# Kernel tuning notes

Measured on AMD Instinct MI355X. Metric: run time of the kernel, lower is better.

The kernel has to match this reference:

```python
import jax, jax.numpy as jnp
import numpy as np

# Brevitas-style fake quantization:
#  - Int8ActPerTensorFloat: signed, symmetric, per-tensor float scale, range [-128, 127]
#  - 4-bit weight, narrow range: [-7, 7]
#  - Int32Bias: quantized at scale s_in * s_w
# Scales are taken from per-tensor abs-max statistics (brevitas stats-based init).

def _round(v):
    return jnp.round(v)

def _fake_quant(v, scale, qmin, qmax):
    return jnp.clip(_round(v / scale), qmin, qmax) * scale


def setup_inputs() -> dict:
    key = jax.random.key(0)
    k1, k2, k3 = jax.random.split(key, 3)
    x = jax.random.normal(k1, (16, 3, 224, 224), dtype=jnp.float32)
    W = jax.random.normal(k2, (128, 3, 3, 3), dtype=jnp.float32) * 0.1
    b = jax.random.normal(k3, (128,), dtype=jnp.float32) * 0.01
    return {"x": x, "W": W, "b": b}


def reference(x, W, b):
    EPS = 1e-8
    # input quant: int8 per-tensor
    s_in = jnp.maximum(jnp.max(jnp.abs(x)) / 127.0, EPS)
    x_q = _fake_quant(x, s_in, -128.0, 127.0)
    # weight quant: 4-bit narrow-range per-tensor
    s_w = jnp.maximum(jnp.max(jnp.abs(W)) / 7.0, EPS)
    w_q = _fake_quant(W, s_w, -7.0, 7.0)
    # bias quant: int32 at scale s_in * s_w
    s_b = s_in * s_w
    b_q = _fake_quant(b, s_b, -2147483648.0, 2147483647.0)
    # conv2d, NCHW x OIHW -> NCHW, stride 1, valid padding (torch default padding=0)
    y = jax.lax.conv_general_dilated(
        x_q, w_q, window_strides=(1, 1), padding="VALID",
        dimension_numbers=("NCHW", "OIHW", "NCHW"))
    y = y + b_q[None, :, None, None]
    # output quant: int8 per-tensor
    s_out = jnp.maximum(jnp.max(jnp.abs(y)) / 127.0, EPS)
    y_q = _fake_quant(y, s_out, -128.0, 127.0)
    return y_q
```

## Files before the change

kernel.cpp:

```cpp
#include <hip/hip_runtime.h>
#include <stdint.h>

#define QEPS 1e-8f

typedef __bf16 bf16x8 __attribute__((ext_vector_type(8)));
typedef unsigned short ushortx8 __attribute__((ext_vector_type(8)));
typedef float floatx4 __attribute__((ext_vector_type(4)));


__global__ void k_init(unsigned int* s) { if (threadIdx.x < 4) s[threadIdx.x] = 0u; }

__global__ __launch_bounds__(256) void k_absmax(
    const float4* __restrict__ x, int n4,
    const float* __restrict__ W, int nw,
    unsigned int* __restrict__ s) {
  __shared__ unsigned int red[256];
  const int t = threadIdx.x;
  unsigned int m = 0u;
  const int i = blockIdx.x * 256 + t;
  if (i < n4) {
    float4 v = x[i];
    m =        __float_as_uint(v.x) & 0x7fffffffu;
    m = max(m, __float_as_uint(v.y) & 0x7fffffffu);
    m = max(m, __float_as_uint(v.z) & 0x7fffffffu);
    m = max(m, __float_as_uint(v.w) & 0x7fffffffu);
  }
  red[t] = m;
  __syncthreads();
  for (int off = 128; off > 0; off >>= 1) {
    if (t < off) red[t] = max(red[t], red[t + off]);
    __syncthreads();
  }
  if (t == 0) atomicMax(&s[0], red[0]);

  if (blockIdx.x == 0) {
    unsigned int mw = 0u;
    for (int j = t; j < nw; j += 256)
      mw = max(mw, __float_as_uint(W[j]) & 0x7fffffffu);
    __syncthreads();
    red[t] = mw;
    __syncthreads();
    for (int off = 128; off > 0; off >>= 1) {
      if (t < off) red[t] = max(red[t], red[t + off]);
      __syncthreads();
    }
    if (t == 0) atomicMax(&s[1], red[0]);
  }
}

#define OFF_XL  8320
#define OFF_QBL 16992
#define OFF_RED 17504
#define OFF_OL  18528
#define SMEM_P0 18528
#define SMEM_P1 47712

template<int PASS>
__global__ __launch_bounds__(256) void k_conv(
    const float* __restrict__ x, const float* __restrict__ W,
    const float* __restrict__ b, float* __restrict__ out,
    unsigned int* __restrict__ s) {
  extern __shared__ __align__(16) char smem[];
  unsigned short* const wl   = (unsigned short*)smem;
  unsigned short* const xl   = (unsigned short*)(smem + OFF_XL);
  float*          const qbl  = (float*)(smem + OFF_QBL);
  float*          const redf = (float*)(smem + OFF_RED);
  unsigned int*   const ol32 = (unsigned int*)(smem + OFF_OL);

  const int t = threadIdx.x;
  const float s_in = fmaxf(__uint_as_float(s[0]) / 127.0f, QEPS);
  const float s_w  = fmaxf(__uint_as_float(s[1]) / 7.0f,  QEPS);
  const float s_b  = s_in * s_w;

  float s_out = 1.0f, h = 1.0f;
  if (PASS == 1) {
    const float vmax = __uint_as_float(s[2]);
    s_out = fmaxf((s_b * vmax) / 127.0f, QEPS);
    h = s_b / s_out;
  }

  for (int i = t; i < 3456; i += 256) {
    const int o = i / 27;
    const int k = i - o * 27;
    float q = rintf(W[i] / s_w);
    q = fminf(fmaxf(q, -7.0f), 7.0f);
    wl[k * 130 + o] = (unsigned short)(__float_as_uint(q) >> 16);
  }
  for (int i = t; i < 5 * 130; i += 256) wl[27 * 130 + i] = 0;
  if (t < 128) qbl[t] = rintf(b[t] / s_b);
  for (int i = t; i < 72; i += 256) xl[(i >> 2) * 228 + 224 + (i & 3)] = 0;
  for (int i = t; i < 228; i += 256) xl[18 * 228 + i] = 0;

  #pragma unroll
  for (int sl = 0; sl < 2; ++sl) {
    const int R = blockIdx.x + sl * 1776;
    const int n = R / 222, oh = R - n * 222;
    for (int i = t; i < 9 * 224; i += 256) {
      const int row = i / 224;
      const int col = i - row * 224;
      const int c = row / 3, kh = row - c * 3;
      const float xv = x[((n * 3 + c) * 224 + (oh + kh)) * 224 + col];
      float q = fminf(fmaxf(rintf(xv / s_in), -128.0f), 127.0f);
      xl[(sl * 9 + row) * 228 + col] = (unsigned short)(__float_as_uint(q) >> 16);
    }
  }
  __syncthreads();

  const int lane = t & 63;
  const int wv = t >> 6;
  const int p = lane & 15;
  const int g = lane >> 4;

  bf16x8 bvw[8];
  #pragma unroll
  for (int tt8 = 0; tt8 < 8; ++tt8) {
    ushortx8 u;
    #pragma unroll
    for (int j = 0; j < 8; ++j)
      u[j] = wl[(g * 8 + j) * 130 + tt8 * 16 + p];
    bvw[tt8] = __builtin_bit_cast(bf16x8, u);
  }
  float qbp[8];
  #pragma unroll
  for (int tt8 = 0; tt8 < 8; ++tt8) qbp[tt8] = qbl[tt8 * 16 + p];

  float vmax_local = 0.0f;

  #pragma unroll
  for (int sl = 0; sl < 2; ++sl) {
    int off2[8];
    #pragma unroll
    for (int j = 0; j < 8; ++j) {
      const int k = g * 8 + j;
      int row, kw;
      if (k < 27) {
        const int c = k / 9, rem = k - c * 9;
        const int kh = rem / 3;
        kw = rem - kh * 3;
        row = sl * 9 + c * 3 + kh;
      } else { row = 18; kw = 0; }
      off2[j] = (row * 228 + kw) * 2;
    }

    const int R = blockIdx.x + sl * 1776;
    const int nn = R / 222, ohh = R - nn * 222;

    #pragma unroll 1
    for (int tt = wv; tt < 14; tt += 4) {
      const int ow0 = tt * 16;
      const char* xbase = (const char*)xl + (ow0 + p) * 2;

      ushortx8 bu;
      #pragma unroll
      for (int j = 0; j < 8; ++j)
        bu[j] = *(const unsigned short*)(xbase + off2[j]);
      const bf16x8 av = __builtin_bit_cast(bf16x8, bu);

      floatx4 acc[8];
      #pragma unroll
      for (int tt8 = 0; tt8 < 8; ++tt8) {
        const float qb = qbp[tt8];
        acc[tt8][0] = qb; acc[tt8][1] = qb; acc[tt8][2] = qb; acc[tt8][3] = qb;
      }
      #pragma unroll
      for (int tt8 = 0; tt8 < 8; ++tt8)
        acc[tt8] = __builtin_amdgcn_mfma_f32_16x16x32_bf16(av, bvw[tt8], acc[tt8], 0, 0, 0);

      if (PASS == 0) {
        #pragma unroll
        for (int tt8 = 0; tt8 < 8; ++tt8)
          #pragma unroll
          for (int r = 0; r < 4; ++r)
            vmax_local = fmaxf(vmax_local,
                (ow0 + 4 * g + r < 222) ? fabsf(acc[tt8][r]) : 0.0f);
      } else {
        #pragma unroll
        for (int tt8 = 0; tt8 < 8; ++tt8) {
          unsigned int pk = 0;
          #pragma unroll
          for (int r = 0; r < 4; ++r) {
            float q = rintf(acc[tt8][r] * h);
            q = fminf(fmaxf(q, -128.0f), 127.0f);
            pk |= ((unsigned int)((int)q & 255)) << (8 * r);
          }
          ol32[(tt8 * 16 + p) * 57 + (ow0 >> 2) + g] = pk;
        }
      }
    }

    if (PASS == 1) {
      __syncthreads();
      #pragma unroll 1
      for (int oc = wv * 32; oc < wv * 32 + 32; ++oc) {
        const unsigned int* src = ol32 + oc * 57;
        float* dst = out + (((nn * 128 + oc) * 222 + ohh) * 222);
        if (lane < 56) {
          const unsigned int bc = src[lane];
          if ((ohh & 1) == 0) {
            float f0 = (float)((int)(bc << 24) >> 24) * s_out;
            float f1 = (float)((int)(bc << 16) >> 24) * s_out;
            float f2 = (float)((int)(bc <<  8) >> 24) * s_out;
            float f3 = (float)((int) bc        >> 24) * s_out;
            if (lane < 55) *(float4*)(dst + 4 * lane) = make_float4(f0, f1, f2, f3);
            else           *(float2*)(dst + 220)      = make_float2(f0, f1);
          } else {
            if (lane == 0) {
              float f0 = (float)((int)(bc << 24) >> 24) * s_out;
              float f1 = (float)((int)(bc << 16) >> 24) * s_out;
              *(float2*)dst = make_float2(f0, f1);
            } else {
              const unsigned int ap = src[lane - 1];
              const unsigned int v = (ap >> 16) | (bc << 16);
              float f0 = (float)((int)(v << 24) >> 24) * s_out;
              float f1 = (float)((int)(v << 16) >> 24) * s_out;
              float f2 = (float)((int)(v <<  8) >> 24) * s_out;
              float f3 = (float)((int) v        >> 24) * s_out;
              *(float4*)(dst + 4 * lane - 2) = make_float4(f0, f1, f2, f3);
            }
          }
        }
      }
      __syncthreads();
    }
  }

  if (PASS == 0) {
    redf[t] = vmax_local;
    __syncthreads();
    for (int off = 128; off > 0; off >>= 1) {
      if (t < off) redf[t] = fmaxf(redf[t], redf[t + off]);
      __syncthreads();
    }
    if (t == 0) atomicMax(&s[2], __float_as_uint(redf[0]));
  }
}

extern "C" void kernel_launch(void* const* d_in, const int* in_sizes, int n_in,
                              void* d_out, int out_size, void* d_ws, size_t ws_size,
                              hipStream_t stream) {
  const float* x = (const float*)d_in[0];
  const float* W = (const float*)d_in[1];
  const float* b = (const float*)d_in[2];
  float* out = (float*)d_out;
  unsigned int* s = (unsigned int*)d_ws;

  k_init<<<1, 64, 0, stream>>>(s);

  const int n4 = in_sizes[0] / 4;
  k_absmax<<<(n4 + 255) / 256, 256, 0, stream>>>(
      (const float4*)x, n4, W, in_sizes[1], s);

  k_conv<0><<<1776, 256, SMEM_P0, stream>>>(x, W, b, out, s);
  k_conv<1><<<1776, 256, SMEM_P1, stream>>>(x, W, b, out, s);
}
```

Measured before the change: 574.1 us.

## Cache int16 conv accumulators in workspace instead of recomputing conv in second pass

```diff
diff --git a/kernel.cpp b/kernel.cpp
--- a/kernel.cpp
+++ b/kernel.cpp
@@ -45,6 +45,189 @@
       __syncthreads();
     }
     if (t == 0) atomicMax(&s[1], red[0]);
+  }
+}
+
+__global__ __launch_bounds__(256) void k_conv_ws(
+    const float* __restrict__ x, const float* __restrict__ W,
+    const float* __restrict__ b, unsigned short* __restrict__ y16,
+    unsigned int* __restrict__ s) {
+  __shared__ __align__(16) unsigned short wl[32 * 130];
+  __shared__ __align__(16) unsigned short xl[19 * 228];
+  __shared__ __align__(16) float qbl[128];
+  __shared__ float redf[256];
+
+  const int t = threadIdx.x;
+  const float s_in = fmaxf(__uint_as_float(s[0]) / 127.0f, QEPS);
+  const float s_w  = fmaxf(__uint_as_float(s[1]) / 7.0f,  QEPS);
+  const float s_b  = s_in * s_w;
+
+  for (int i = t; i < 3456; i += 256) {
+    const int o = i / 27;
+    const int k = i - o * 27;
+    float q = rintf(W[i] / s_w);
+    q = fminf(fmaxf(q, -7.0f), 7.0f);
+    wl[k * 130 + o] = (unsigned short)(__float_as_uint(q) >> 16);
+  }
+  for (int i = t; i < 5 * 130; i += 256) wl[27 * 130 + i] = 0;
+  if (t < 128) qbl[t] = rintf(b[t] / s_b);
+  for (int i = t; i < 72; i += 256) xl[(i >> 2) * 228 + 224 + (i & 3)] = 0;
+  for (int i = t; i < 228; i += 256) xl[18 * 228 + i] = 0;
+
+  #pragma unroll
+  for (int sl = 0; sl < 2; ++sl) {
+    const int R = blockIdx.x + sl * 1776;
+    const int n = R / 222, oh = R - n * 222;
+    for (int i = t; i < 9 * 224; i += 256) {
+      const int row = i / 224;
+      const int col = i - row * 224;
+      const int c = row / 3, kh = row - c * 3;
+      const float xv = x[((n * 3 + c) * 224 + (oh + kh)) * 224 + col];
+      float q = fminf(fmaxf(rintf(xv / s_in), -128.0f), 127.0f);
+      xl[(sl * 9 + row) * 228 + col] = (unsigned short)(__float_as_uint(q) >> 16);
+    }
+  }
+  __syncthreads();
+
+  const int lane = t & 63;
+  const int wv = t >> 6;
+  const int p = lane & 15;
+  const int g = lane >> 4;
+
+  bf16x8 bvw[8];
+  #pragma unroll
+  for (int tt8 = 0; tt8 < 8; ++tt8) {
+    ushortx8 u;
+    #pragma unroll
+    for (int j = 0; j < 8; ++j)
+      u[j] = wl[(g * 8 + j) * 130 + tt8 * 16 + p];
+    bvw[tt8] = __builtin_bit_cast(bf16x8, u);
+  }
+  float qbp[8];
+  #pragma unroll
+  for (int tt8 = 0; tt8 < 8; ++tt8) qbp[tt8] = qbl[tt8 * 16 + p];
+
+  float vmax_local = 0.0f;
+
+  #pragma unroll
+  for (int sl = 0; sl < 2; ++sl) {
+    int off2[8];
+    #pragma unroll
+    for (int j = 0; j < 8; ++j) {
+      const int k = g * 8 + j;
+      int row, kw;
+      if (k < 27) {
+        const int c = k / 9, rem = k - c * 9;
+        const int kh = rem / 3;
+        kw = rem - kh * 3;
+        row = sl * 9 + c * 3 + kh;
+      } else { row = 18; kw = 0; }
+      off2[j] = (row * 228 + kw) * 2;
+    }
+
+    const int R = blockIdx.x + sl * 1776;
+    unsigned short* yrow = y16 + (size_t)R * 28672;
+
+    #pragma unroll 1
+    for (int tt = wv; tt < 14; tt += 4) {
+      const int ow0 = tt * 16;
+      const char* xbase = (const char*)xl + (ow0 + p) * 2;
+
+      ushortx8 bu;
+      #pragma unroll
+      for (int j = 0; j < 8; ++j)
+        bu[j] = *(const unsigned short*)(xbase + off2[j]);
+      const bf16x8 av = __builtin_bit_cast(bf16x8, bu);
+
+      floatx4 acc[8];
+      #pragma unroll
+      for (int tt8 = 0; tt8 < 8; ++tt8) {
+        const float qb = qbp[tt8];
+        acc[tt8][0] = qb; acc[tt8][1] = qb; acc[tt8][2] = qb; acc[tt8][3] = qb;
+      }
+      #pragma unroll
+      for (int tt8 = 0; tt8 < 8; ++tt8)
+        acc[tt8] = __builtin_amdgcn_mfma_f32_16x16x32_bf16(av, bvw[tt8], acc[tt8], 0, 0, 0);
+
+      #pragma unroll
+      for (int tt8 = 0; tt8 < 8; ++tt8) {
+        const int a0 = (int)acc[tt8][0], a1 = (int)acc[tt8][1];
+        const int a2 = (int)acc[tt8][2], a3 = (int)acc[tt8][3];
+        uint2 pk;
+        pk.x = ((unsigned)a0 & 0xffffu) | ((unsigned)a1 << 16);
+        pk.y = ((unsigned)a2 & 0xffffu) | ((unsigned)a3 << 16);
+        *(uint2*)(yrow + (tt8 * 16 + p) * 224 + ow0 + 4 * g) = pk;
+        #pragma unroll
+        for (int r = 0; r < 4; ++r)
+          vmax_local = fmaxf(vmax_local,
+              (ow0 + 4 * g + r < 222) ? fabsf(acc[tt8][r]) : 0.0f);
+      }
+    }
+  }
+
+  redf[t] = vmax_local;
+  __syncthreads();
+  for (int off = 128; off > 0; off >>= 1) {
+    if (t < off) redf[t] = fmaxf(redf[t], redf[t + off]);
+    __syncthreads();
+  }
+  if (t == 0) atomicMax(&s[2], __float_as_uint(redf[0]));
+}
+
+__global__ __launch_bounds__(256) void k_final(
+    const unsigned short* __restrict__ y16, float* __restrict__ out,
+    const unsigned int* __restrict__ s) {
+  const float s_in = fmaxf(__uint_as_float(s[0]) / 127.0f, QEPS);
+  const float s_w  = fmaxf(__uint_as_float(s[1]) / 7.0f,  QEPS);
+  const float s_b  = s_in * s_w;
+  const float vmax = __uint_as_float(s[2]);
+  const float s_out = fmaxf((s_b * vmax) / 127.0f, QEPS);
+  const float h = s_b / s_out;
+
+  const int R = blockIdx.x;
+  const int nn = R / 222, ohh = R - nn * 222;
+  const int t = threadIdx.x, lane = t & 63, wv = t >> 6;
+  const int* srcrow = (const int*)(y16 + (size_t)R * 28672);
+
+  #pragma unroll 1
+  for (int oc = wv * 32; oc < wv * 32 + 32; ++oc) {
+    const int* src = srcrow + oc * 112;
+    float* dst = out + ((size_t)(nn * 128 + oc) * 222 + ohh) * 222;
+    if (lane < 56) {
+      if ((ohh & 1) == 0) {
+        const int2 d = *(const int2*)(src + 2 * lane);
+        float f0 = (float)(short)(d.x & 0xffff);
+        float f1 = (float)(short)(d.x >> 16);
+        float f2 = (float)(short)(d.y & 0xffff);
+        float f3 = (float)(short)(d.y >> 16);
+        f0 = fminf(fmaxf(rintf(f0 * h), -128.0f), 127.0f) * s_out;
+        f1 = fminf(fmaxf(rintf(f1 * h), -128.0f), 127.0f) * s_out;
+        f2 = fminf(fmaxf(rintf(f2 * h), -128.0f), 127.0f) * s_out;
+        f3 = fminf(fmaxf(rintf(f3 * h), -128.0f), 127.0f) * s_out;
+        if (lane < 55) *(float4*)(dst + 4 * lane) = make_float4(f0, f1, f2, f3);
+        else           *(float2*)(dst + 220)      = make_float2(f0, f1);
+      } else {
+        if (lane == 0) {
+          const int d0 = src[0];
+          float f0 = (float)(short)(d0 & 0xffff);
+          float f1 = (float)(short)(d0 >> 16);
+          f0 = fminf(fmaxf(rintf(f0 * h), -128.0f), 127.0f) * s_out;
+          f1 = fminf(fmaxf(rintf(f1 * h), -128.0f), 127.0f) * s_out;
+          *(float2*)dst = make_float2(f0, f1);
+        } else {
+          const int da = src[2 * lane - 1], db = src[2 * lane];
+          float f0 = (float)(short)(da & 0xffff);
+          float f1 = (float)(short)(da >> 16);
+          float f2 = (float)(short)(db & 0xffff);
+          float f3 = (float)(short)(db >> 16);
+          f0 = fminf(fmaxf(rintf(f0 * h), -128.0f), 127.0f) * s_out;
+          f1 = fminf(fmaxf(rintf(f1 * h), -128.0f), 127.0f) * s_out;
+          f2 = fminf(fmaxf(rintf(f2 * h), -128.0f), 127.0f) * s_out;
+          f3 = fminf(fmaxf(rintf(f3 * h), -128.0f), 127.0f) * s_out;
+          *(float4*)(dst + 4 * lane - 2) = make_float4(f0, f1, f2, f3);
+        }
+      }
+    }
   }
 }
 
@@ -250,6 +433,13 @@
   k_absmax<<<(n4 + 255) / 256, 256, 0, stream>>>(
       (const float4*)x, n4, W, in_sizes[1], s);
 
-  k_conv<0><<<1776, 256, SMEM_P0, stream>>>(x, W, b, out, s);
-  k_conv<1><<<1776, 256, SMEM_P1, stream>>>(x, W, b, out, s);
+  const size_t WS_NEED = 256ull + 3552ull * 57344ull;
+  if (ws_size >= WS_NEED) {
+    unsigned short* y16 = (unsigned short*)((char*)d_ws + 256);
+    k_conv_ws<<<1776, 256, 0, stream>>>(x, W, b, y16, s);
+    k_final<<<3552, 256, 0, stream>>>(y16, out, s);
+  } else {
+    k_conv<0><<<1776, 256, SMEM_P0, stream>>>(x, W, b, out, s);
+    k_conv<1><<<1776, 256, SMEM_P1, stream>>>(x, W, b, out, s);
+  }
 }
```

Result: slower. 630.4 us (+9.8%).
